# Optimization experiments

Hardware: AMD Instinct MI355X
Metric: run time of the kernel (lower is better)

Reference implementation:

```python
import jax, jax.numpy as jnp
import numpy as np

KATZ = 0.5      # katz_factor
GAMMA = 20.0    # support->query softmax temperature
GAMMA2 = 10.0   # query->support softmax temperature
EPS = 1e-16


def setup_inputs() -> dict:
    key = jax.random.key(0)
    k1, k2 = jax.random.split(key)
    support_xf = jax.random.normal(k1, (4, 25, 640, 10, 10), dtype=jnp.float32)
    query_xf = jax.random.normal(k2, (4, 75, 640, 10, 10), dtype=jnp.float32)
    return {"support_xf": support_xf, "query_xf": query_xf, "n_way": 5, "k_shot": 5}


def reference(support_xf, query_xf, n_way, k_shot):
    b, s, c, h, w = support_xf.shape
    q = query_xf.shape[1]
    M = h * w
    # mean over shots -> class prototypes per spatial location
    sup = support_xf.reshape(b, n_way, k_shot, c, M).mean(axis=2)   # (b, n, c, M)
    qry = query_xf.reshape(b, q, c, M)                               # (b, q, c, M)
    # cosine similarity: l2-normalize along channel dim
    sup = sup / (EPS + jnp.linalg.norm(sup, axis=2, keepdims=True))
    qry = qry / (EPS + jnp.linalg.norm(qry, axis=2, keepdims=True))
    # S[b,q,m,n,s] = <qry[b,q,:,m], sup[b,n,:,s]>  (matches permute(0,1,3,2,4))
    S = jnp.einsum('bqcm,bncs->bqmns', qry, sup)
    M_q = M
    M_s = n_way * M
    N = b * q
    S = S.reshape(N, M_q, M_s)
    # bipartite transition matrices (row-stochastic softmaxes)
    T_sq = jax.nn.softmax(GAMMA * S, axis=-1)                        # (N, M_q, M_s)
    T_qs = jax.nn.softmax(GAMMA2 * jnp.swapaxes(S, -2, -1), axis=-1)  # (N, M_s, M_q)
    D = M_s + M_q
    zs = jnp.zeros((N, M_s, M_s), S.dtype)
    zq = jnp.zeros((N, M_q, M_q), S.dtype)
    top = jnp.concatenate([zs, jnp.swapaxes(T_sq, -2, -1)], axis=-1)   # (N, M_s, D)
    bot = jnp.concatenate([jnp.swapaxes(T_qs, -2, -1), zq], axis=-1)   # (N, M_q, D)
    T = jnp.concatenate([top, bot], axis=-2)                           # (N, D, D)
    # katz = (inv(I - k*T) - I) @ 1  ==  solve(I - k*T, 1) - 1
    A = jnp.eye(D, dtype=S.dtype)[None] - KATZ * T
    katz = jnp.linalg.solve(A, jnp.ones((N, D, 1), S.dtype))[..., 0] - 1.0
    kq = katz[:, M_s:]
    kq = kq / kq.sum(axis=-1, keepdims=True)
    return kq.reshape(b, q, h, w)[:, :, None]  # (b, q, 1, h, w)
```

## Files before the change

### kernel.cpp

```cpp
#include <hip/hip_runtime.h>
#include <math.h>

#define BATCH 4
#define NSUP 25
#define NQ   75
#define CH   640
#define HW   100
#define NWAY 5
#define KSHOT 5
#define NSYS (BATCH*NQ)
#define MS   (NWAY*HW)
#define MQ   HW
#define MTOT (NQ*HW)
#define NCHK 20

#define A_BSTRIDE 241664
#define A_KSTRIDE 966656
#define B_BSTRIDE 16384
#define B_KSTRIDE 65536

typedef __attribute__((ext_vector_type(8))) _Float16 f16x8;
typedef __attribute__((ext_vector_type(8))) short bf16x8;
typedef __attribute__((ext_vector_type(4))) float f32x4;
typedef __attribute__((ext_vector_type(16))) float f32x16;
typedef __attribute__((ext_vector_type(4))) short s16x4;

__device__ __forceinline__ ushort f2bf(float f) {
    unsigned u = __float_as_uint(f);
    u += 0x7fff + ((u >> 16) & 1);
    return (ushort)(u >> 16);
}
__device__ __forceinline__ ushort f2h(float f) {
    _Float16 h = (_Float16)f;
    return __builtin_bit_cast(unsigned short, h);
}

#define GLD_LDS16(gp, lp) __builtin_amdgcn_global_load_lds( \
    (const __attribute__((address_space(1))) unsigned*)(const void*)(gp), \
    (__attribute__((address_space(3))) unsigned*)(void*)(lp), 16, 0, 0)

__global__ __launch_bounds__(256) void k_prep_all(
        const float* __restrict__ qry, const float* __restrict__ sup,
        ushort* __restrict__ AhT, ushort* __restrict__ BhT,
        float* __restrict__ npq, float* __restrict__ nps) {
    __shared__ float tile[32][101];
    int kt = blockIdx.x;
    int c0 = kt * 32;
    int z  = blockIdx.y;
    int t  = threadIdx.x;
    bool isq = (z < BATCH*NQ);

    ushort* dst; float* normpart; int planesHW; size_t cbase; int brow; int p;
    if (isq) {
        p = z;
        int b = p / NQ, qq = p % NQ;
        dst = AhT; normpart = npq; planesHW = NSYS*HW;
        cbase = (size_t)kt*A_KSTRIDE + (size_t)b*A_BSTRIDE;
        brow = qq*100;
        const float* ib = qry + (size_t)p*CH*HW + (size_t)c0*HW;
#pragma unroll
        for (int ii = 0; ii < 4; ++ii) {
            int idx = ii*256 + t;
            if (idx < 800) {
                int cl = idx / 25, qd = idx % 25;
                float4 v = *(const float4*)(ib + idx*4);
                tile[cl][qd*4+0] = v.x; tile[cl][qd*4+1] = v.y;
                tile[cl][qd*4+2] = v.z; tile[cl][qd*4+3] = v.w;
            }
        }
    } else {
        p = z - BATCH*NQ;
        int b = p / NWAY, n = p % NWAY;
        dst = BhT; normpart = nps; planesHW = BATCH*NWAY*HW;
        cbase = (size_t)kt*B_KSTRIDE + (size_t)b*B_BSTRIDE;
        brow = n*100;
        const float* ib = sup + ((size_t)(b*NSUP + n*KSHOT))*CH*HW + (size_t)c0*HW;
#pragma unroll
        for (int ii = 0; ii < 4; ++ii) {
            int idx = ii*256 + t;
            if (idx < 800) {
                float4 a = {0.f,0.f,0.f,0.f};
#pragma unroll
                for (int k = 0; k < KSHOT; ++k) {
                    float4 w = *(const float4*)(ib + (size_t)k*CH*HW + idx*4);
                    a.x += w.x; a.y += w.y; a.z += w.z; a.w += w.w;
                }
                int cl = idx / 25, qd = idx % 25;
                tile[cl][qd*4+0] = a.x*0.2f; tile[cl][qd*4+1] = a.y*0.2f;
                tile[cl][qd*4+2] = a.z*0.2f; tile[cl][qd*4+3] = a.w*0.2f;
            }
        }
    }
    __syncthreads();
#pragma unroll
    for (int ii = 0; ii < 2; ++ii) {
        int idx = ii*256 + t;
        if (idx < 400) {
            int m  = idx >> 2;
            int sp = idx & 3;
            int rib = brow + m;
            int rl = rib & 127;
            int slab = rib >> 7;
            int cb = ((sp ^ ((rl >> 1) & 3))) << 3;
            bf16x8 o; float ss = 0.f;
#pragma unroll
            for (int j = 0; j < 8; ++j) {
                float f = tile[cb+j][m];
                ss += f*f;
                o[j] = (short)f2h(f);
            }
            size_t off = cbase + (size_t)slab*4096
                       + (size_t)((rl>>1)*64 + (rl&1)*32 + sp*8);
            *(bf16x8*)(dst + off) = o;
            ss += __shfl_xor(ss, 1);
            ss += __shfl_xor(ss, 2);
            if ((t & 3) == 0)
                normpart[(size_t)kt*planesHW + p*HW + m] = ss;
        }
    }
}

#define BM 128
#define BN 128
#define BK 64
#define NKT (CH/BK)
#define NCT 4
#define NRT 59
#define NWG (NCT*NRT*BATCH)
__global__ __launch_bounds__(256) void k_gemm(
        const ushort* __restrict__ AhT, const ushort* __restrict__ BhT,
        const float* __restrict__ npq, const float* __restrict__ nps,
        float* __restrict__ S) {
    __shared__ __align__(1024) char lds[65536];
    __shared__ float invqL[128], invsL[128];
    int hwid = blockIdx.x;
    int l = (hwid & 7) * (NWG/8) + (hwid >> 3);
    int ct = l & 3;
    int rest = l >> 2;
    int rt = rest % NRT;
    int b  = rest / NRT;
    int t  = threadIdx.x;
    int lane = t & 63, w = t >> 6;
    int row0 = rt * BM, col0 = ct * BN;

    if (t < 128) {
        int gr = row0 + t; if (gr > MTOT-1) gr = MTOT-1;
        float s = 0.f;
#pragma unroll
        for (int u = 0; u < NCHK; ++u) s += npq[(size_t)u*(NSYS*HW) + b*MTOT + gr];
        invqL[t] = 1.0f / (1e-16f + sqrtf(s));
    } else {
        int c = col0 + (t - 128); if (c > MS-1) c = MS-1;
        float s = 0.f;
#pragma unroll
        for (int u = 0; u < NCHK; ++u) s += nps[(size_t)u*(BATCH*NWAY*HW) + b*MS + c];
        invsL[t-128] = 1.0f / (1e-16f + sqrtf(s));
    }

    const ushort* srcA = AhT + (size_t)b*A_BSTRIDE + (size_t)rt*4096;
    const ushort* srcB = BhT + (size_t)b*B_BSTRIDE + (size_t)ct*4096;
    int dA = w << 10;

    f32x4 acc[4][4];
#pragma unroll
    for (int mi = 0; mi < 4; ++mi)
#pragma unroll
        for (int ni = 0; ni < 4; ++ni) acc[mi][ni] = (f32x4){0.f,0.f,0.f,0.f};

    int wr = w >> 1, wc = w & 1;
    int q = lane & 15, kg = lane >> 4;

#define STAGE(bufb, kt_) do { \
        const ushort* pa0 = srcA + (size_t)(2*(kt_))*A_KSTRIDE; \
        const ushort* pa1 = pa0 + A_KSTRIDE; \
        const ushort* pb0 = srcB + (size_t)(2*(kt_))*B_KSTRIDE; \
        const ushort* pb1 = pb0 + B_KSTRIDE; \
        char* bb = lds + (bufb)*32768; \
        GLD_LDS16(pa0 + t*8,        bb + 0     + dA); \
        GLD_LDS16(pa0 + 2048 + t*8, bb + 4096  + dA); \
        GLD_LDS16(pa1 + t*8,        bb + 8192  + dA); \
        GLD_LDS16(pa1 + 2048 + t*8, bb + 12288 + dA); \
        GLD_LDS16(pb0 + t*8,        bb + 16384 + dA); \
        GLD_LDS16(pb0 + 2048 + t*8, bb + 20480 + dA); \
        GLD_LDS16(pb1 + t*8,        bb + 24576 + dA); \
        GLD_LDS16(pb1 + 2048 + t*8, bb + 28672 + dA); \
    } while (0)

    STAGE(0, 0);
    for (int kt = 0; kt < NKT; ++kt) {
        int cur = kt & 1;
        if (kt + 1 < NKT) {
            STAGE(cur ^ 1, kt + 1);
            asm volatile("s_waitcnt vmcnt(8)" ::: "memory");
        } else {
            asm volatile("s_waitcnt vmcnt(0)" ::: "memory");
        }
        __builtin_amdgcn_sched_barrier(0);
        __builtin_amdgcn_s_barrier();
        __builtin_amdgcn_sched_barrier(0);

        const char* buf = lds + cur*32768;
#pragma unroll
        for (int h = 0; h < 2; ++h) {
            const char* Ab = buf + h*8192;
            const char* Bb = buf + 16384 + h*8192;
            f16x8 bf[4];
#pragma unroll
            for (int ni = 0; ni < 4; ++ni) {
                int c = wc*64 + ni*16 + q;
                int off = (c>>1)*128 + (c&1)*64 + ((kg ^ ((c>>1)&3)) << 4);
                bf[ni] = *(const f16x8*)(Bb + off);
            }
#pragma unroll
            for (int mi = 0; mi < 4; ++mi) {
                int r = wr*64 + mi*16 + q;
                int off = (r>>1)*128 + (r&1)*64 + ((kg ^ ((r>>1)&3)) << 4);
                f16x8 af = *(const f16x8*)(Ab + off);
#pragma unroll
                for (int ni = 0; ni < 4; ++ni)
                    acc[mi][ni] = __builtin_amdgcn_mfma_f32_16x16x32_f16(af, bf[ni], acc[mi][ni], 0, 0, 0);
            }
        }
        __builtin_amdgcn_sched_barrier(0);
        __builtin_amdgcn_s_barrier();
        __builtin_amdgcn_sched_barrier(0);
    }
#undef STAGE

    int colb = col0 + wc*64 + q;
    int rowb = row0 + wr*64 + (kg << 2);
#pragma unroll
    for (int mi = 0; mi < 4; ++mi) {
#pragma unroll
        for (int ni = 0; ni < 4; ++ni) {
            int c = colb + ni*16;
            if (c >= MS) continue;
            float si = invsL[c - col0];
#pragma unroll
            for (int j = 0; j < 4; ++j) {
                int r = rowb + mi*16 + j;
                if (r < MTOT)
                    S[((size_t)b*MTOT + r)*MS + c] = acc[mi][ni][j] * invqL[r - row0] * si;
            }
        }
    }
}

__global__ __launch_bounds__(512) void k_fsolve(const float* __restrict__ S,
        float* __restrict__ out) {
    __shared__ __align__(16) char PQ[65536];
    __shared__ __align__(16) float r10s[MS];
    __shared__ float r20L[MQ];
    __shared__ float xs[MQ], ys[MQ], rh[MQ];
    __shared__ float ps[4][MQ];
    __shared__ float partial[2];
    int sys = blockIdx.x;
    int t = threadIdx.x;
    int l = t & 63, w = t >> 6;
    const float* Sb = S + (size_t)sys*MQ*MS;
    char* PT = PQ;
    char* QT = PQ + 32768;

    {
        float (*wcs)[512] = (float(*)[512])PQ;
        float cols[8];
#pragma unroll
        for (int u = 0; u < 8; ++u) cols[u] = 0.f;
        int nu = (l < MS - 448) ? 8 : 7;
        for (int row = w; row < MQ; row += 8) {
            const float* rp = Sb + (size_t)row*MS;
#pragma unroll
            for (int u = 0; u < 8; ++u)
                if (u < nu) cols[u] += __expf(10.f*(rp[l + 64*u] - 1.0f));
        }
#pragma unroll
        for (int u = 0; u < 8; ++u) wcs[w][l+64*u] = cols[u];
        __syncthreads();
        if (t < MS) {
            float s = 0.f;
#pragma unroll
            for (int w2 = 0; w2 < 8; ++w2) s += wcs[w2][t];
            r10s[t] = 1.0f/s;
        }
    }

    int i = t >> 2;
    int ccb = (t & 3) * 32;

    f32x16 acc[2];
#pragma unroll
    for (int nt = 0; nt < 2; ++nt)
#pragma unroll
        for (int rg = 0; rg < 16; ++rg) acc[nt][rg] = 0.f;

    int rw = w & 3, ch = w >> 2;
    int grA = rw*32 + (l & 31);
    int kg = l >> 5;
    const float* sr = Sb + (size_t)i*MS;

    for (int ck = 0; ck < 4; ++ck) {
        int c0 = ck*128;
        __syncthreads();
        if (i < MQ) {
#pragma unroll
            for (int j = 0; j < 8; ++j) {
                int cc = ccb + 4*j;
                int cg = c0 + cc;
                int phys = i*256 + ((((cc>>3) ^ (i&15)))<<4) + ((cc&7)*2);
                s16x4 pv, qv;
                if (cg < MS) {
                    float4 v  = *(const float4*)(sr + cg);
                    float4 r1 = *(const float4*)&r10s[cg];
                    pv.x = (short)f2bf(__expf(10.f*(v.x - 1.0f))*r1.x);
                    pv.y = (short)f2bf(__expf(10.f*(v.y - 1.0f))*r1.y);
                    pv.z = (short)f2bf(__expf(10.f*(v.z - 1.0f))*r1.z);
                    pv.w = (short)f2bf(__expf(10.f*(v.w - 1.0f))*r1.w);
                    qv.x = (short)f2bf(__expf(20.f*(v.x - 1.0f)));
                    qv.y = (short)f2bf(__expf(20.f*(v.y - 1.0f)));
                    qv.z = (short)f2bf(__expf(20.f*(v.z - 1.0f)));
                    qv.w = (short)f2bf(__expf(20.f*(v.w - 1.0f)));
                } else {
                    pv = (s16x4){0,0,0,0}; qv = (s16x4){0,0,0,0};
                }
                *(s16x4*)(PT + phys) = pv;
                *(s16x4*)(QT + phys) = qv;
            }
        } else {
            short one = (short)0x3F80;
#pragma unroll
            for (int j = 0; j < 8; ++j) {
                int cc = ccb + 4*j;
                int cg = c0 + cc;
                int phys = i*256 + ((((cc>>3) ^ (i&15)))<<4) + ((cc&7)*2);
                s16x4 z = (s16x4){0,0,0,0};
                s16x4 ov = z;
                if (i == MQ && cg < MS) ov = (s16x4){one, one, one, one};
                *(s16x4*)(PT + phys) = ov;
                *(s16x4*)(QT + phys) = ov;
            }
        }
        __syncthreads();
#pragma unroll
        for (int kk = 0; kk < 8; ++kk) {
            int sA = (kk*2 + kg) ^ (grA & 15);
            bf16x8 af = *(const bf16x8*)(PT + grA*256 + (sA<<4));
#pragma unroll
            for (int nt = 0; nt < 2; ++nt) {
                int gc = (ch*2 + nt)*32 + (l & 31);
                int sB = (kk*2 + kg) ^ (gc & 15);
                bf16x8 bfr = *(const bf16x8*)(QT + gc*256 + (sB<<4));
                acc[nt] = __builtin_amdgcn_mfma_f32_32x32x16_bf16(af, bfr, acc[nt], 0, 0, 0);
            }
        }
    }
    __syncthreads();

    float* Bsh = (float*)PQ;
#pragma unroll
    for (int nt = 0; nt < 2; ++nt) {
        int col = (ch*2 + nt)*32 + (l & 31);
        if (col > MQ) continue;
#pragma unroll
        for (int rg = 0; rg < 16; ++rg) {
            int row = rw*32 + (rg & 3) + 8*(rg >> 2) + 4*(l >> 5);
            if (row <= MQ) Bsh[row*101 + col] = acc[nt][rg];
        }
    }
    __syncthreads();
    if (t < MQ) {
        float r20 = 1.0f / Bsh[100*101 + t];
        r20L[t] = r20;
        float r = 1.0f + 0.5f*Bsh[t*101 + 100];
        rh[t] = r;
        xs[t] = r;
        ys[t] = r20 * r;
    }
    __syncthreads();
    int jr = t % MQ, jp = t / MQ;
    for (int it = 0; it < 12; ++it) {
        if (t < 4*MQ) {
            float s = 0.f;
            const float* br = &Bsh[jr*101 + jp*25];
            const float* yv = &ys[jp*25];
#pragma unroll
            for (int j = 0; j < 25; ++j) s += br[j]*yv[j];
            ps[jp][jr] = s;
        }
        __syncthreads();
        if (t < MQ) {
            float x = rh[t] + 0.25f*(ps[0][t] + ps[1][t] + ps[2][t] + ps[3][t]);
            xs[t] = x;
            ys[t] = r20L[t] * x;
        }
        __syncthreads();
    }
    float kv = (t < MQ) ? (xs[t] - 1.0f) : 0.f;
    if (t < 128) {
        float s = kv;
        for (int off = 32; off; off >>= 1) s += __shfl_xor(s, off);
        if ((t & 63) == 0) partial[t >> 6] = s;
    }
    __syncthreads();
    float tot = partial[0] + partial[1];
    if (t < MQ) out[sys*MQ + t] = kv / tot;
}

extern "C" void kernel_launch(void* const* d_in, const int* in_sizes, int n_in,
                              void* d_out, int out_size, void* d_ws, size_t ws_size,
                              hipStream_t stream) {
    const float* sup = (const float*)d_in[0];
    const float* qry = (const float*)d_in[1];
    float* out = (float*)d_out;
    float* ws  = (float*)d_ws;

    float* supmean = ws;
    float* invs    = supmean + 1280000;
    float* invq    = invs + 2000;
    float* Smat    = invq + 30000;
    float* m20     = Smat + 15000000;
    float* rd20    = m20 + 30000;
    float* m10     = rd20 + 30000;
    float* rd10    = m10 + 150000;
    float* Bm      = rd10 + 150000;
    float* rh      = Bm + 3000000;
    ushort* AhT    = (ushort*)(rh + 30000);
    ushort* BhT    = AhT + 19333120;
    float* npq     = Bm;
    float* nps     = Bm + 600000;

    k_prep_all<<<dim3(NCHK, BATCH*NQ + BATCH*NWAY), 256, 0, stream>>>(
        qry, sup, AhT, BhT, npq, nps);
    k_gemm<<<NWG, 256, 0, stream>>>(AhT, BhT, npq, nps, Smat);
    k_fsolve<<<NSYS, 512, 0, stream>>>(Smat, out);
}
```

Measured before the change: 112.0 us.

## Fuse column exp-sum for query softmax into GEMM epilogue

```diff
diff --git a/kernel.cpp b/kernel.cpp
--- a/kernel.cpp
+++ b/kernel.cpp
@@ -130,9 +130,10 @@
 __global__ __launch_bounds__(256) void k_gemm(
         const ushort* __restrict__ AhT, const ushort* __restrict__ BhT,
         const float* __restrict__ npq, const float* __restrict__ nps,
-        float* __restrict__ S) {
+        float* __restrict__ S, float* __restrict__ pcs) {
     __shared__ __align__(1024) char lds[65536];
     __shared__ float invqL[128], invsL[128];
+    __shared__ float csL[384];
     int hwid = blockIdx.x;
     int l = (hwid & 7) * (NWG/8) + (hwid >> 3);
     int ct = l & 3;
@@ -156,6 +157,8 @@
         for (int u = 0; u < NCHK; ++u) s += nps[(size_t)u*(BATCH*NWAY*HW) + b*MS + c];
         invsL[t-128] = 1.0f / (1e-16f + sqrtf(s));
     }
+    if (t < 384 - 256) csL[256 + t] = 0.f;
+    csL[t] = 0.f;
 
     const ushort* srcA = AhT + (size_t)b*A_BSTRIDE + (size_t)rt*4096;
     const ushort* srcB = BhT + (size_t)b*B_BSTRIDE + (size_t)ct*4096;
@@ -229,25 +232,42 @@
 
     int colb = col0 + wc*64 + q;
     int rowb = row0 + wr*64 + (kg << 2);
-#pragma unroll
-    for (int mi = 0; mi < 4; ++mi) {
-#pragma unroll
-        for (int ni = 0; ni < 4; ++ni) {
-            int c = colb + ni*16;
-            if (c >= MS) continue;
-            float si = invsL[c - col0];
+    int sys0 = row0 / 100;
+    int segb = rowb / 100 - sys0;
+    int rowcross = (rowb/100 + 1) * 100;
+#pragma unroll
+    for (int ni = 0; ni < 4; ++ni) {
+        int c = colb + ni*16;
+        if (c >= MS) continue;
+        float si = invsL[c - col0];
+        float s0 = 0.f, s1 = 0.f;
+#pragma unroll
+        for (int mi = 0; mi < 4; ++mi) {
 #pragma unroll
             for (int j = 0; j < 4; ++j) {
                 int r = rowb + mi*16 + j;
-                if (r < MTOT)
-                    S[((size_t)b*MTOT + r)*MS + c] = acc[mi][ni][j] * invqL[r - row0] * si;
-            }
-        }
+                if (r < MTOT) {
+                    float v = acc[mi][ni][j] * invqL[r - row0] * si;
+                    S[((size_t)b*MTOT + r)*MS + c] = v;
+                    float e = __expf(10.f*(v - 1.0f));
+                    if (r < rowcross) s0 += e; else s1 += e;
+                }
+            }
+        }
+        atomicAdd(&csL[segb*128 + (c - col0)], s0);
+        if (s1 != 0.f) atomicAdd(&csL[(segb+1)*128 + (c - col0)], s1);
+    }
+    __syncthreads();
+    for (int z = t; z < 384; z += 256) {
+        int seg = z >> 7, cl = z & 127;
+        int c = col0 + cl;
+        if (c < MS)
+            pcs[((size_t)(b*NRT + rt)*3 + seg)*512 + c] = csL[z];
     }
 }
 
 __global__ __launch_bounds__(512) void k_fsolve(const float* __restrict__ S,
-        float* __restrict__ out) {
+        const float* __restrict__ pcs, float* __restrict__ out) {
     __shared__ __align__(16) char PQ[65536];
     __shared__ __align__(16) float r10s[MS];
     __shared__ float r20L[MQ];
@@ -262,25 +282,20 @@
     char* QT = PQ + 32768;
 
     {
-        float (*wcs)[512] = (float(*)[512])PQ;
-        float cols[8];
-#pragma unroll
-        for (int u = 0; u < 8; ++u) cols[u] = 0.f;
-        int nu = (l < MS - 448) ? 8 : 7;
-        for (int row = w; row < MQ; row += 8) {
-            const float* rp = Sb + (size_t)row*MS;
-#pragma unroll
-            for (int u = 0; u < 8; ++u)
-                if (u < nu) cols[u] += __expf(10.f*(rp[l + 64*u] - 1.0f));
-        }
-#pragma unroll
-        for (int u = 0; u < 8; ++u) wcs[w][l+64*u] = cols[u];
-        __syncthreads();
-        if (t < MS) {
-            float s = 0.f;
-#pragma unroll
-            for (int w2 = 0; w2 < 8; ++w2) s += wcs[w2][t];
-            r10s[t] = 1.0f/s;
+        int bq = sys / NQ, qq = sys % NQ;
+        int rt1 = (qq*100) >> 7;
+        int rt2 = (qq*100 + 99) >> 7;
+        int seg1 = qq - (rt1*128)/100;
+        const float* p1 = pcs + ((size_t)(bq*NRT + rt1)*3 + seg1)*512;
+        const float* p2 = nullptr;
+        if (rt2 != rt1) {
+            int seg2 = qq - (rt2*128)/100;
+            p2 = pcs + ((size_t)(bq*NRT + rt2)*3 + seg2)*512;
+        }
+        for (int c = t; c < MS; c += 512) {
+            float s = p1[c];
+            if (p2) s += p2[c];
+            r10s[c] = 1.0f/s;
         }
     }
 
@@ -427,9 +442,10 @@
     ushort* BhT    = AhT + 19333120;
     float* npq     = Bm;
     float* nps     = Bm + 600000;
+    float* pcs     = Bm + 640000;
 
     k_prep_all<<<dim3(NCHK, BATCH*NQ + BATCH*NWAY), 256, 0, stream>>>(
         qry, sup, AhT, BhT, npq, nps);
-    k_gemm<<<NWG, 256, 0, stream>>>(AhT, BhT, npq, nps, Smat);
-    k_fsolve<<<NSYS, 512, 0, stream>>>(Smat, out);
-}
+    k_gemm<<<NWG, 256, 0, stream>>>(AhT, BhT, npq, nps, Smat, pcs);
+    k_fsolve<<<NSYS, 512, 0, stream>>>(Smat, pcs, out);
+}
```

Result: slower. 114.5 us (+2.2%).
